# Performance work log

Measured on AMD Instinct MI355X. Metric: run time of the kernel, lower is better.

## Reference

```python
import jax, jax.numpy as jnp
import numpy as np

B, S, DIN, DOUT = 4, 2048, 4096, 4096
QMAX = 7  # int4 symmetric: values in [-8, 7]

def setup_inputs() -> dict:
    key = jax.random.key(0)
    kx, kq, ks, kb = jax.random.split(key, 4)
    x = jax.random.normal(kx, (B, S, DIN), dtype=jnp.float32)
    # int4 codes stored as int32, symmetric per-output-channel quantization
    qweight = jax.random.randint(kq, (DOUT, DIN), -8, 8, dtype=jnp.int32)
    # per-output-channel scale (max_abs / 7 style), strictly positive
    scale = jax.random.uniform(ks, (DOUT,), dtype=jnp.float32, minval=0.005, maxval=0.02)
    bias = jax.random.normal(kb, (DOUT,), dtype=jnp.float32)
    return {"x": x, "qweight": qweight, "scale": scale, "bias": bias}

def reference(x, qweight, scale, bias):
    # dequantize: per-output-channel scale broadcast over in_features
    weight = qweight.astype(jnp.float32) * scale[:, None]  # [DOUT, DIN]
    # F.linear: x @ weight.T + bias
    return jnp.einsum('bsi,oi->bso', x, weight) + bias
```

## Files before the change

### kernel.cpp

```cpp
#include <hip/hip_runtime.h>

typedef unsigned short u16;
typedef unsigned int u32;
typedef unsigned char u8;

typedef int i32x4 __attribute__((ext_vector_type(4)));
typedef float f32x4 __attribute__((ext_vector_type(4)));

#define AS1 __attribute__((address_space(1)))
#define AS3 __attribute__((address_space(3)))

__global__ __launch_bounds__(256) void quant_x_kernel(
    const float* __restrict__ x, u8* __restrict__ xq, float* __restrict__ sx, int K)
{
    const int r = blockIdx.x;
    const int t = threadIdx.x;
    const float* xr = x + (size_t)r * K;
    float4 v[4];
    float m = 0.f;
#pragma unroll
    for (int i = 0; i < 4; ++i) {
        v[i] = *(const float4*)(xr + t * 16 + i * 4);
        m = fmaxf(m, fmaxf(fmaxf(fabsf(v[i].x), fabsf(v[i].y)),
                           fmaxf(fabsf(v[i].z), fabsf(v[i].w))));
    }
#pragma unroll
    for (int s = 32; s; s >>= 1) m = fmaxf(m, __shfl_xor(m, s));
    __shared__ float wm[4];
    if ((t & 63) == 0) wm[t >> 6] = m;
    __syncthreads();
    m = fmaxf(fmaxf(wm[0], wm[1]), fmaxf(wm[2], wm[3]));
    const float inv = 127.f / fmaxf(m, 1e-20f);
    if (t == 0) sx[r] = m * (1.f / 127.f);
    u32 o[4];
#pragma unroll
    for (int i = 0; i < 4; ++i) {
        int q0 = (int)rintf(v[i].x * inv), q1 = (int)rintf(v[i].y * inv);
        int q2 = (int)rintf(v[i].z * inv), q3 = (int)rintf(v[i].w * inv);
        o[i] = (u32)(q0 & 255) | ((u32)(q1 & 255) << 8) |
               ((u32)(q2 & 255) << 16) | ((u32)(q3 & 255) << 24);
    }
    *(uint4*)(xq + (size_t)r * K + t * 16) = make_uint4(o[0], o[1], o[2], o[3]);
}

__device__ __forceinline__ u32 pk8(int4 a) {
    return (u32)(a.x & 255) | ((u32)(a.y & 255) << 8) |
           ((u32)(a.z & 255) << 16) | ((u32)(a.w & 255) << 24);
}

__global__ void quant_w_kernel(const int4* __restrict__ q, uint4* __restrict__ y, int n16) {
    int stride = gridDim.x * blockDim.x;
    for (int i = blockIdx.x * blockDim.x + threadIdx.x; i < n16; i += stride) {
        int4 a = q[4 * i], b = q[4 * i + 1], c = q[4 * i + 2], d = q[4 * i + 3];
        y[i] = make_uint4(pk8(a), pk8(b), pk8(c), pk8(d));
    }
}


#define BM 256
#define BN 256
#define BKB 128

template<int KS, int MLO, bool GATE, typename F>
__device__ __forceinline__ void phase(const char* aB, const char* bB,
    i32x4 (&bfr)[2][4], i32x4 (&acc)[8][4], F&& stage)
{
    stage();
    i32x4 afr[4];
    if (MLO == 0) {
#pragma unroll
        for (int fn = 0; fn < 4; ++fn)
            bfr[KS][fn] = *(const i32x4*)(bB + fn * 2048);
    }
#pragma unroll
    for (int fm = 0; fm < 4; ++fm)
        afr[fm] = *(const i32x4*)(aB + (MLO + fm) * 2048);
    __builtin_amdgcn_s_setprio(1);
#pragma unroll
    for (int fm = 0; fm < 4; ++fm)
#pragma unroll
        for (int fn = 0; fn < 4; ++fn)
            acc[MLO + fm][fn] = __builtin_amdgcn_mfma_i32_16x16x64_i8(
                bfr[KS][fn], afr[fm], acc[MLO + fm][fn], 0, 0, 0);
    __builtin_amdgcn_s_setprio(0);
    if (GATE) asm volatile("s_waitcnt vmcnt(4)" ::: "memory");
    __builtin_amdgcn_s_barrier();
}

__global__ __launch_bounds__(512, 2) void gemm256_i8(
    const u8* __restrict__ A,
    const u8* __restrict__ W,
    const float* __restrict__ sx,
    const float* __restrict__ scale,
    const float* __restrict__ bias,
    float* __restrict__ C,
    int M, int N, int K)
{
    __shared__ alignas(1024) char lds[131072];

    const int nwg = gridDim.x;
    int bid = blockIdx.x;
    if ((nwg & 7) == 0) { int cpx = nwg >> 3; bid = (bid & 7) * cpx + (bid >> 3); }
    const int ntn = N / BN;
    const int tm = bid / ntn, tn = bid % ntn;

    const int t = threadIdx.x;
    const int l = t & 63;
    const int w = t >> 6;
    const int wm = w >> 2, wn = w & 3;
    const size_t Kz = (size_t)K;

    const int sRow = t >> 3;
    const int sCol = (((t & 7) ^ ((t >> 3) & 7)) * 16);
    const u8* aSrc = A + (size_t)(tm * BM + sRow) * Kz + sCol;
    const u8* bSrc = W + (size_t)(tn * BN + sRow) * Kz + sCol;
    const int wByte = w * 1024;

    char* dA0 = lds + wByte;
    char* dB0 = lds + 32768 + wByte;
    char* dA1 = lds + 65536 + wByte;
    char* dB1 = lds + 98304 + wByte;

    const int rowA = (wm * 128 + (l & 15)) * 128;
    const int rowB = (wn * 64  + (l & 15)) * 128;
    const int sl0 = (((l >> 4) | 0) ^ (l & 7)) * 16;
    const int sl1 = (((l >> 4) | 4) ^ (l & 7)) * 16;

    const char* aX0 = lds +         rowA + sl0;
    const char* aX1 = lds +         rowA + sl1;
    const char* bX0 = lds + 32768 + rowB + sl0;
    const char* bX1 = lds + 32768 + rowB + sl1;
    const char* aY0 = lds + 65536 + rowA + sl0;
    const char* aY1 = lds + 65536 + rowA + sl1;
    const char* bY0 = lds + 98304 + rowB + sl0;
    const char* bY1 = lds + 98304 + rowB + sl1;

    i32x4 acc[8][4];
#pragma unroll
    for (int i = 0; i < 8; ++i)
#pragma unroll
        for (int j = 0; j < 4; ++j) acc[i][j] = (i32x4){0, 0, 0, 0};

    const int NT = K / BKB;

    auto stagePair = [&](const u8* src, char* dst, int kt, int c0, int c1) {
        const u8* s0 = src + (size_t)c0 * 64 * Kz + (size_t)kt * BKB;
        const u8* s1 = src + (size_t)c1 * 64 * Kz + (size_t)kt * BKB;
        __builtin_amdgcn_global_load_lds((const AS1 void*)s0, (AS3 void*)(dst + c0 * 8192), 16, 0, 0);
        __builtin_amdgcn_global_load_lds((const AS1 void*)s1, (AS3 void*)(dst + c1 * 8192), 16, 0, 0);
    };

    stagePair(aSrc, dA0, 0, 0, 2);
    stagePair(bSrc, dB0, 0, 0, 1);
    stagePair(bSrc, dB0, 0, 2, 3);
    stagePair(aSrc, dA0, 0, 1, 3);
    stagePair(bSrc, dB1, 1, 0, 1);
    stagePair(bSrc, dB1, 1, 2, 3);
    asm volatile("s_waitcnt vmcnt(4)" ::: "memory");
    __builtin_amdgcn_s_barrier();

    i32x4 bfr[2][4];

#pragma unroll 1
    for (int i = 0; i < NT / 2; ++i) {
        const int yt = 2 * i + 1;
        const int e  = (2 * i + 2) & (NT - 1);
        const int o  = (2 * i + 3) & (NT - 1);
        phase<0, 0, false>(aX0, bX0, bfr, acc, [&] { stagePair(aSrc, dA1, yt, 0, 2); });
        phase<1, 0, false>(aX1, bX1, bfr, acc, [&] { stagePair(aSrc, dA1, yt, 1, 3); });
        phase<0, 4, false>(aX0, bX0, bfr, acc, [&] { stagePair(aSrc, dA0, e, 0, 2); });
        phase<1, 4, true >(aX1, bX1, bfr, acc, [&] { stagePair(bSrc, dB0, e, 0, 1); });
        phase<0, 0, false>(aY0, bY0, bfr, acc, [&] { stagePair(bSrc, dB0, e, 2, 3); });
        phase<1, 0, false>(aY1, bY1, bfr, acc, [&] { stagePair(aSrc, dA0, e, 1, 3); });
        phase<0, 4, false>(aY0, bY0, bfr, acc, [&] { stagePair(bSrc, dB1, o, 0, 1); });
        phase<1, 4, true >(aY1, bY1, bfr, acc, [&] { stagePair(bSrc, dB1, o, 2, 3); });
    }

    const int mB = tm * BM + wm * 128 + (l & 15);
    const int nB = tn * BN + wn * 64 + 4 * (l >> 4);
    float sxv[8];
#pragma unroll
    for (int f = 0; f < 8; ++f) sxv[f] = sx[mB + f * 16];
#pragma unroll
    for (int fn = 0; fn < 4; ++fn) {
        const int n0 = nB + fn * 16;
        const float4 s4 = *(const float4*)(scale + n0);
        const float4 b4 = *(const float4*)(bias + n0);
#pragma unroll
        for (int f = 0; f < 8; ++f) {
            const int m = mB + f * 16;
            const float sm = sxv[f];
            float4 v;
            v.x = (float)acc[f][fn][0] * (sm * s4.x) + b4.x;
            v.y = (float)acc[f][fn][1] * (sm * s4.y) + b4.y;
            v.z = (float)acc[f][fn][2] * (sm * s4.z) + b4.z;
            v.w = (float)acc[f][fn][3] * (sm * s4.w) + b4.w;
            *(float4*)(C + (size_t)m * N + n0) = v;
        }
    }
}

extern "C" void kernel_launch(void* const* d_in, const int* in_sizes, int n_in,
                              void* d_out, int out_size, void* d_ws, size_t ws_size,
                              hipStream_t stream) {
    const float* x     = (const float*)d_in[0];
    const int*   qw    = (const int*)d_in[1];
    const float* scale = (const float*)d_in[2];
    const float* bias  = (const float*)d_in[3];
    float*       out   = (float*)d_out;

    const int N = in_sizes[2];
    const int K = in_sizes[1] / N;
    const int M = in_sizes[0] / K;

    u8*    xq = (u8*)d_ws;
    u8*    wq = xq + (size_t)M * K;
    float* sx = (float*)(wq + (size_t)N * K);

    quant_x_kernel<<<M, 256, 0, stream>>>(x, xq, sx, K);
    quant_w_kernel<<<2048, 256, 0, stream>>>((const int4*)qw, (uint4*)wq, (N * K) / 16);

    const int grid = (M / BM) * (N / BN);
    gemm256_i8<<<grid, 512, 0, stream>>>(xq, wq, sx, scale, bias, out, M, N, K);
}
```

Measured before the change: 180.1 us.

## Software-pipeline LDS fragment reads one phase ahead of MFMA compute

Restructures the GEMM main loop so each phase loads the next phase's A and B fragments from LDS into a second register set while issuing MFMAs on the current set, double-buffering the A fragments. The global-to-LDS staging order and the vmcnt gate thresholds are reshuffled to match, and an lgkmcnt(0) wait is added before each barrier. This aims to hide LDS read latency behind matrix-core work. It costs extra VGPRs under a 2-waves-per-SIMD launch bound, and the hand-tuned staging and wait counts are fragile.

```diff
diff --git a/kernel.cpp b/kernel.cpp
--- a/kernel.cpp
+++ b/kernel.cpp
@@ -61,29 +61,31 @@
 #define BN 256
 #define BKB 128
 
-template<int KS, int MLO, bool GATE, typename F>
-__device__ __forceinline__ void phase(const char* aB, const char* bB,
+template<int KSC, int MLOC, bool RDB, int BS, bool GATE, typename F>
+__device__ __forceinline__ void phaseRA(
+    const char* aN, const char* bN, int mloN,
+    i32x4 (&afrC)[4], i32x4 (&afrN)[4],
     i32x4 (&bfr)[2][4], i32x4 (&acc)[8][4], F&& stage)
 {
     stage();
-    i32x4 afr[4];
-    if (MLO == 0) {
+    if (RDB) {
 #pragma unroll
         for (int fn = 0; fn < 4; ++fn)
-            bfr[KS][fn] = *(const i32x4*)(bB + fn * 2048);
-    }
-#pragma unroll
-    for (int fm = 0; fm < 4; ++fm)
-        afr[fm] = *(const i32x4*)(aB + (MLO + fm) * 2048);
+            bfr[BS][fn] = *(const i32x4*)(bN + fn * 2048);
+    }
+#pragma unroll
+    for (int f = 0; f < 4; ++f)
+        afrN[f] = *(const i32x4*)(aN + (mloN + f) * 2048);
     __builtin_amdgcn_s_setprio(1);
 #pragma unroll
-    for (int fm = 0; fm < 4; ++fm)
+    for (int f = 0; f < 4; ++f)
 #pragma unroll
         for (int fn = 0; fn < 4; ++fn)
-            acc[MLO + fm][fn] = __builtin_amdgcn_mfma_i32_16x16x64_i8(
-                bfr[KS][fn], afr[fm], acc[MLO + fm][fn], 0, 0, 0);
+            acc[MLOC + f][fn] = __builtin_amdgcn_mfma_i32_16x16x64_i8(
+                bfr[KSC][fn], afrC[f], acc[MLOC + f][fn], 0, 0, 0);
     __builtin_amdgcn_s_setprio(0);
-    if (GATE) asm volatile("s_waitcnt vmcnt(4)" ::: "memory");
+    asm volatile("s_waitcnt lgkmcnt(0)" ::: "memory");
+    if (GATE) asm volatile("s_waitcnt vmcnt(2)" ::: "memory");
     __builtin_amdgcn_s_barrier();
 }
 
@@ -154,26 +156,41 @@
     stagePair(bSrc, dB0, 0, 0, 1);
     stagePair(bSrc, dB0, 0, 2, 3);
     stagePair(aSrc, dA0, 0, 1, 3);
+    stagePair(aSrc, dA1, 1, 0, 2);
     stagePair(bSrc, dB1, 1, 0, 1);
-    stagePair(bSrc, dB1, 1, 2, 3);
     asm volatile("s_waitcnt vmcnt(4)" ::: "memory");
     __builtin_amdgcn_s_barrier();
 
     i32x4 bfr[2][4];
+    i32x4 afrA[4], afrB[4];
+#pragma unroll
+    for (int fn = 0; fn < 4; ++fn)
+        bfr[0][fn] = *(const i32x4*)(bX0 + fn * 2048);
+#pragma unroll
+    for (int f = 0; f < 4; ++f)
+        afrA[f] = *(const i32x4*)(aX0 + f * 2048);
 
 #pragma unroll 1
     for (int i = 0; i < NT / 2; ++i) {
         const int yt = 2 * i + 1;
         const int e  = (2 * i + 2) & (NT - 1);
         const int o  = (2 * i + 3) & (NT - 1);
-        phase<0, 0, false>(aX0, bX0, bfr, acc, [&] { stagePair(aSrc, dA1, yt, 0, 2); });
-        phase<1, 0, false>(aX1, bX1, bfr, acc, [&] { stagePair(aSrc, dA1, yt, 1, 3); });
-        phase<0, 4, false>(aX0, bX0, bfr, acc, [&] { stagePair(aSrc, dA0, e, 0, 2); });
-        phase<1, 4, true >(aX1, bX1, bfr, acc, [&] { stagePair(bSrc, dB0, e, 0, 1); });
-        phase<0, 0, false>(aY0, bY0, bfr, acc, [&] { stagePair(bSrc, dB0, e, 2, 3); });
-        phase<1, 0, false>(aY1, bY1, bfr, acc, [&] { stagePair(aSrc, dA0, e, 1, 3); });
-        phase<0, 4, false>(aY0, bY0, bfr, acc, [&] { stagePair(bSrc, dB1, o, 0, 1); });
-        phase<1, 4, true >(aY1, bY1, bfr, acc, [&] { stagePair(bSrc, dB1, o, 2, 3); });
+        phaseRA<0, 0, true , 1, false>(aX1, bX1, 0, afrA, afrB, bfr, acc,
+            [&] { stagePair(aSrc, dA1, yt, 1, 3); });
+        phaseRA<1, 0, false, 0, false>(aX0, bX0, 4, afrB, afrA, bfr, acc,
+            [&] { stagePair(bSrc, dB1, yt, 2, 3); });
+        phaseRA<0, 4, false, 0, true >(aX1, bX1, 4, afrA, afrB, bfr, acc,
+            [&] { stagePair(aSrc, dA0, e, 0, 2); });
+        phaseRA<1, 4, true , 0, false>(aY0, bY0, 0, afrB, afrA, bfr, acc,
+            [&] { stagePair(bSrc, dB0, e, 0, 1); });
+        phaseRA<0, 0, true , 1, false>(aY1, bY1, 0, afrA, afrB, bfr, acc,
+            [&] { stagePair(aSrc, dA0, e, 1, 3); });
+        phaseRA<1, 0, false, 0, false>(aY0, bY0, 4, afrB, afrA, bfr, acc,
+            [&] { stagePair(bSrc, dB0, e, 2, 3); });
+        phaseRA<0, 4, false, 0, true >(aY1, bY1, 4, afrA, afrB, bfr, acc,
+            [&] { stagePair(aSrc, dA1, o, 0, 2); });
+        phaseRA<1, 4, true , 0, false>(aX0, bX0, 0, afrB, afrA, bfr, acc,
+            [&] { stagePair(bSrc, dB1, o, 0, 1); });
     }
 
     const int mB = tm * BM + wm * 128 + (l & 15);
```

Measured after the change: 177.9 us, median of 2. Within noise of the previous version (-1.3%).

## Restructure int8 GEMM to 4 waves with 128x128 warp tiles and register double-buffering

Applied to the files above, without the earlier changes.

Moves the 256x256 int8 GEMM tile from 8 waves (128x64 per wave) to 4 waves (128x128 per wave), so each wave holds 8x8 accumulators and reuses more LDS fragments per MFMA. The 8-phase fine-grained staging schedule is replaced by whole-tile staging with register ping-pong fragments and full waitcnt/barrier gates twice per tile pair. This cuts LDS reads per FLOP and sync count. The cost is very high register pressure from 256 accumulator VGPRs plus 64 fragment registers, fewer waves to hide latency, and coarser vmcnt(0) waits that expose global load latency.

```diff
diff --git a/kernel.cpp b/kernel.cpp
--- a/kernel.cpp
+++ b/kernel.cpp
@@ -5,7 +5,6 @@
 typedef unsigned char u8;
 
 typedef int i32x4 __attribute__((ext_vector_type(4)));
-typedef float f32x4 __attribute__((ext_vector_type(4)));
 
 #define AS1 __attribute__((address_space(1)))
 #define AS3 __attribute__((address_space(3)))
@@ -61,33 +60,7 @@
 #define BN 256
 #define BKB 128
 
-template<int KS, int MLO, bool GATE, typename F>
-__device__ __forceinline__ void phase(const char* aB, const char* bB,
-    i32x4 (&bfr)[2][4], i32x4 (&acc)[8][4], F&& stage)
-{
-    stage();
-    i32x4 afr[4];
-    if (MLO == 0) {
-#pragma unroll
-        for (int fn = 0; fn < 4; ++fn)
-            bfr[KS][fn] = *(const i32x4*)(bB + fn * 2048);
-    }
-#pragma unroll
-    for (int fm = 0; fm < 4; ++fm)
-        afr[fm] = *(const i32x4*)(aB + (MLO + fm) * 2048);
-    __builtin_amdgcn_s_setprio(1);
-#pragma unroll
-    for (int fm = 0; fm < 4; ++fm)
-#pragma unroll
-        for (int fn = 0; fn < 4; ++fn)
-            acc[MLO + fm][fn] = __builtin_amdgcn_mfma_i32_16x16x64_i8(
-                bfr[KS][fn], afr[fm], acc[MLO + fm][fn], 0, 0, 0);
-    __builtin_amdgcn_s_setprio(0);
-    if (GATE) asm volatile("s_waitcnt vmcnt(4)" ::: "memory");
-    __builtin_amdgcn_s_barrier();
-}
-
-__global__ __launch_bounds__(512, 2) void gemm256_i8(
+__global__ __launch_bounds__(256, 1) void gemm256_i8(
     const u8* __restrict__ A,
     const u8* __restrict__ W,
     const float* __restrict__ sx,
@@ -107,7 +80,7 @@
     const int t = threadIdx.x;
     const int l = t & 63;
     const int w = t >> 6;
-    const int wm = w >> 2, wn = w & 3;
+    const int wm = w >> 1, wn = w & 1;
     const size_t Kz = (size_t)K;
 
     const int sRow = t >> 3;
@@ -116,73 +89,98 @@
     const u8* bSrc = W + (size_t)(tn * BN + sRow) * Kz + sCol;
     const int wByte = w * 1024;
 
-    char* dA0 = lds + wByte;
+    char* dA0 = lds +      0 + wByte;
     char* dB0 = lds + 32768 + wByte;
     char* dA1 = lds + 65536 + wByte;
     char* dB1 = lds + 98304 + wByte;
 
     const int rowA = (wm * 128 + (l & 15)) * 128;
-    const int rowB = (wn * 64  + (l & 15)) * 128;
+    const int rowB = (wn * 128 + (l & 15)) * 128;
     const int sl0 = (((l >> 4) | 0) ^ (l & 7)) * 16;
     const int sl1 = (((l >> 4) | 4) ^ (l & 7)) * 16;
 
-    const char* aX0 = lds +         rowA + sl0;
-    const char* aX1 = lds +         rowA + sl1;
-    const char* bX0 = lds + 32768 + rowB + sl0;
-    const char* bX1 = lds + 32768 + rowB + sl1;
-    const char* aY0 = lds + 65536 + rowA + sl0;
-    const char* aY1 = lds + 65536 + rowA + sl1;
-    const char* bY0 = lds + 98304 + rowB + sl0;
-    const char* bY1 = lds + 98304 + rowB + sl1;
-
-    i32x4 acc[8][4];
+    const char* aBase0 = lds +      0 + rowA;
+    const char* bBase0 = lds + 32768 + rowB;
+    const char* aBase1 = lds + 65536 + rowA;
+    const char* bBase1 = lds + 98304 + rowB;
+
+    i32x4 acc[8][8];
 #pragma unroll
     for (int i = 0; i < 8; ++i)
 #pragma unroll
-        for (int j = 0; j < 4; ++j) acc[i][j] = (i32x4){0, 0, 0, 0};
+        for (int j = 0; j < 8; ++j) acc[i][j] = (i32x4){0, 0, 0, 0};
 
     const int NT = K / BKB;
 
-    auto stagePair = [&](const u8* src, char* dst, int kt, int c0, int c1) {
-        const u8* s0 = src + (size_t)c0 * 64 * Kz + (size_t)kt * BKB;
-        const u8* s1 = src + (size_t)c1 * 64 * Kz + (size_t)kt * BKB;
-        __builtin_amdgcn_global_load_lds((const AS1 void*)s0, (AS3 void*)(dst + c0 * 8192), 16, 0, 0);
-        __builtin_amdgcn_global_load_lds((const AS1 void*)s1, (AS3 void*)(dst + c1 * 8192), 16, 0, 0);
+    auto stageTile = [&](char* dstA, char* dstB, int kt) {
+#pragma unroll
+        for (int c = 0; c < 8; ++c)
+            __builtin_amdgcn_global_load_lds(
+                (const AS1 void*)(aSrc + (size_t)c * 32 * Kz + (size_t)kt * BKB),
+                (AS3 void*)(dstA + c * 4096), 16, 0, 0);
+#pragma unroll
+        for (int c = 0; c < 8; ++c)
+            __builtin_amdgcn_global_load_lds(
+                (const AS1 void*)(bSrc + (size_t)c * 32 * Kz + (size_t)kt * BKB),
+                (AS3 void*)(dstB + c * 4096), 16, 0, 0);
     };
-
-    stagePair(aSrc, dA0, 0, 0, 2);
-    stagePair(bSrc, dB0, 0, 0, 1);
-    stagePair(bSrc, dB0, 0, 2, 3);
-    stagePair(aSrc, dA0, 0, 1, 3);
-    stagePair(bSrc, dB1, 1, 0, 1);
-    stagePair(bSrc, dB1, 1, 2, 3);
-    asm volatile("s_waitcnt vmcnt(4)" ::: "memory");
+    auto readF = [&](i32x4 (&dst)[8], const char* base, int sl) {
+#pragma unroll
+        for (int f = 0; f < 8; ++f)
+            dst[f] = *(const i32x4*)(base + f * 2048 + sl);
+    };
+    auto mfma64 = [&](i32x4 (&bf)[8], i32x4 (&af)[8]) {
+#pragma unroll
+        for (int f = 0; f < 8; ++f)
+#pragma unroll
+            for (int fn = 0; fn < 8; ++fn)
+                acc[f][fn] = __builtin_amdgcn_mfma_i32_16x16x64_i8(
+                    bf[fn], af[f], acc[f][fn], 0, 0, 0);
+    };
+
+#define SYNC_GATE  do { \
+    asm volatile("s_waitcnt lgkmcnt(0)" ::: "memory"); \
+    asm volatile("s_waitcnt vmcnt(0)"  ::: "memory"); \
+    __builtin_amdgcn_s_barrier(); } while (0)
+
+    stageTile(dA0, dB0, 0);
+    stageTile(dA1, dB1, 1);
+    asm volatile("s_waitcnt vmcnt(16)" ::: "memory");
     __builtin_amdgcn_s_barrier();
 
-    i32x4 bfr[2][4];
+    i32x4 afrP[8], bfrP[8], afrQ[8], bfrQ[8];
+    readF(afrP, aBase0, sl0);
+    readF(bfrP, bBase0, sl0);
 
 #pragma unroll 1
     for (int i = 0; i < NT / 2; ++i) {
-        const int yt = 2 * i + 1;
-        const int e  = (2 * i + 2) & (NT - 1);
-        const int o  = (2 * i + 3) & (NT - 1);
-        phase<0, 0, false>(aX0, bX0, bfr, acc, [&] { stagePair(aSrc, dA1, yt, 0, 2); });
-        phase<1, 0, false>(aX1, bX1, bfr, acc, [&] { stagePair(aSrc, dA1, yt, 1, 3); });
-        phase<0, 4, false>(aX0, bX0, bfr, acc, [&] { stagePair(aSrc, dA0, e, 0, 2); });
-        phase<1, 4, true >(aX1, bX1, bfr, acc, [&] { stagePair(bSrc, dB0, e, 0, 1); });
-        phase<0, 0, false>(aY0, bY0, bfr, acc, [&] { stagePair(bSrc, dB0, e, 2, 3); });
-        phase<1, 0, false>(aY1, bY1, bfr, acc, [&] { stagePair(aSrc, dA0, e, 1, 3); });
-        phase<0, 4, false>(aY0, bY0, bfr, acc, [&] { stagePair(bSrc, dB1, o, 0, 1); });
-        phase<1, 4, true >(aY1, bY1, bfr, acc, [&] { stagePair(bSrc, dB1, o, 2, 3); });
+        const int tE2 = (2 * i + 2) & (NT - 1);
+        const int tO2 = (2 * i + 3) & (NT - 1);
+        mfma64(bfrP, afrP);
+        readF(afrQ, aBase0, sl1);
+        readF(bfrQ, bBase0, sl1);
+        SYNC_GATE;
+        mfma64(bfrQ, afrQ);
+        readF(afrP, aBase1, sl0);
+        readF(bfrP, bBase1, sl0);
+        stageTile(dA0, dB0, tE2);
+        mfma64(bfrP, afrP);
+        readF(afrQ, aBase1, sl1);
+        readF(bfrQ, bBase1, sl1);
+        SYNC_GATE;
+        mfma64(bfrQ, afrQ);
+        readF(afrP, aBase0, sl0);
+        readF(bfrP, bBase0, sl0);
+        stageTile(dA1, dB1, tO2);
     }
 
     const int mB = tm * BM + wm * 128 + (l & 15);
-    const int nB = tn * BN + wn * 64 + 4 * (l >> 4);
+    const int nB = tn * BN + wn * 128 + 4 * (l >> 4);
     float sxv[8];
 #pragma unroll
     for (int f = 0; f < 8; ++f) sxv[f] = sx[mB + f * 16];
 #pragma unroll
-    for (int fn = 0; fn < 4; ++fn) {
+    for (int fn = 0; fn < 8; ++fn) {
         const int n0 = nB + fn * 16;
         const float4 s4 = *(const float4*)(scale + n0);
         const float4 b4 = *(const float4*)(bias + n0);
@@ -198,6 +196,7 @@
             *(float4*)(C + (size_t)m * N + n0) = v;
         }
     }
+#undef SYNC_GATE
 }
 
 extern "C" void kernel_launch(void* const* d_in, const int* in_sizes, int n_in,
@@ -221,5 +220,5 @@
     quant_w_kernel<<<2048, 256, 0, stream>>>((const int4*)qw, (uint4*)wq, (N * K) / 16);
 
     const int grid = (M / BM) * (N / BN);
-    gemm256_i8<<<grid, 512, 0, stream>>>(xq, wq, sx, scale, bias, out, M, N, K);
-}
+    gemm256_i8<<<grid, 256, 0, stream>>>(xq, wq, sx, scale, bias, out, M, N, K);
+}
```

Measured after the change: 217.6 us. 20.8% more time.
